# Kernel optimization log

Measured on AMD Instinct MI355X. Metric: run time of the kernel, lower is better.

The kernel has to match this reference:

```python
import jax, jax.numpy as jnp
import numpy as np

D_MODEL = 1024
N_HEADS = 16
D_HEAD = D_MODEL // N_HEADS
B, T = 2, 2048


def setup_inputs() -> dict:
    key = jax.random.key(0)
    k1, k2, k3 = jax.random.split(key, 3)
    x = jax.random.normal(k1, (B, T, D_MODEL), dtype=jnp.float32)
    # torch nn.Linear weights: y = x @ W.T, W has shape [out, in]
    W_qkv = jax.random.normal(k2, (3 * D_MODEL, D_MODEL), dtype=jnp.float32) * (1.0 / np.sqrt(D_MODEL))
    W_out = jax.random.normal(k3, (D_MODEL, D_MODEL), dtype=jnp.float32) * (1.0 / np.sqrt(D_MODEL))
    return {"x": x, "W_qkv": W_qkv, "W_out": W_out}


def reference(x, W_qkv, W_out):
    Bb, Tt, Dd = x.shape
    qkv = (x @ W_qkv.T).reshape(Bb, Tt, 3, N_HEADS, D_HEAD)
    q, k, v = qkv[:, :, 0], qkv[:, :, 1], qkv[:, :, 2]  # [B,T,H,d]
    q = q.transpose(0, 2, 1, 3)  # [B,H,T,d]
    k = k.transpose(0, 2, 1, 3)
    v = v.transpose(0, 2, 1, 3)
    scale = 1.0 / np.sqrt(D_HEAD)
    scores = jnp.einsum('bhqd,bhkd->bhqk', q, k) * scale  # [B,H,T,T]
    causal = jnp.tril(jnp.ones((Tt, Tt), dtype=bool))
    scores = jnp.where(causal, scores, -jnp.inf)
    A = jax.nn.softmax(scores, axis=-1)
    AV = jnp.einsum('bhqk,bhkd->bhqd', A, v)
    AAV = jnp.einsum('bhqk,bhkd->bhqd', A, AV)  # twicing correction
    out = 2.0 * AV - AAV  # [B,H,T,d]
    out = out.transpose(0, 2, 1, 3).reshape(Bb, Tt, Dd)
    return out @ W_out.T
```

## Files before the change

### kernel.cpp

```cpp
#include <hip/hip_runtime.h>
#include <hip/hip_bf16.h>

#define T_SEQ  2048
#define DMODEL 1024
#define NH     16
#define DH     64
#define NTOK   4096
#define QSCALE 0.18033688011112042f
#define M_FIX  16.0f

typedef unsigned short u16;
typedef short s16x8 __attribute__((ext_vector_type(8)));
typedef unsigned short u16x8 __attribute__((ext_vector_type(8)));
typedef float f32x4 __attribute__((ext_vector_type(4)));

__device__ __forceinline__ u16 f2bf(float f) {
  unsigned u = __float_as_uint(f);
  u += 0x7FFFu + ((u >> 16) & 1u);
  return (u16)(u >> 16);
}
__device__ __forceinline__ unsigned pk2(float a, float b) {
  __hip_bfloat162 h = __float22bfloat162_rn(make_float2(a, b));
  unsigned u;
  __builtin_memcpy(&u, &h, 4);
  return u;
}
__device__ __forceinline__ unsigned pk2z(float a, float b) {
  return __builtin_amdgcn_perm(__float_as_uint(b), __float_as_uint(a), 0x07060302);
}
__device__ __forceinline__ float bf2f(u16 x) {
  return __uint_as_float(((unsigned)x) << 16);
}
__device__ __forceinline__ void async_cp16(const u16* g, u16* l) {
  __builtin_amdgcn_global_load_lds(
      (const __attribute__((address_space(1))) unsigned*)g,
      (__attribute__((address_space(3))) unsigned*)l, 16, 0, 0);
}

__global__ void cast_all(const float* __restrict__ x, const float* __restrict__ wqkv,
                         const float* __restrict__ wout, u16* __restrict__ out) {
  int i = blockIdx.x * blockDim.x + threadIdx.x;
  const float* src; int off;
  if (i < 1048576)      { src = x;    off = 0; }
  else if (i < 1835008) { src = wqkv; off = 1048576; }
  else                  { src = wout; off = 1835008; }
  float4 v = reinterpret_cast<const float4*>(src)[i - off];
  ushort4 r;
  r.x = f2bf(v.x); r.y = f2bf(v.y); r.z = f2bf(v.z); r.w = f2bf(v.w);
  reinterpret_cast<ushort4*>(out)[i] = r;
}

__global__ __launch_bounds__(512, 2) void gemm_qkv(
    const u16* __restrict__ A, const u16* __restrict__ Bm,
    u16* __restrict__ outQ, u16* __restrict__ outK, u16* __restrict__ outV) {
  __shared__ __align__(16) u16 SM[57344];
  const int tid = threadIdx.x, wave = tid >> 6, lane = tid & 63;
  const int f15 = lane & 15, quad = lane >> 4;
  const int bm = blockIdx.x * 256, bn = blockIdx.y * 192;
  const int wm = wave >> 2, wn = wave & 3;
  const int K = DMODEL;

  f32x4 acc[8][3] = {};

  const u16* Ag0 = A + (size_t)(bm + (2 * wave) * 16 + f15) * K + quad * 8;
  const u16* Ag1 = A + (size_t)(bm + (2 * wave + 1) * 16 + f15) * K + quad * 8;
  const int bf0 = (wave < 4) ? (2 * wave) : (wave + 4);
  const int bf1 = 2 * wave + 1;
  const u16* Bg0 = Bm + (size_t)(bn + bf0 * 16 + f15) * K + quad * 8;
  const u16* Bg1 = Bm + (size_t)(bn + bf1 * 16 + f15) * K + quad * 8;
  u16* LA0 = SM + (2 * wave) * 512 + lane * 8;
  u16* LA1 = SM + (2 * wave + 1) * 512 + lane * 8;
  u16* LB0 = SM + 8192 + bf0 * 512 + lane * 8;
  u16* LB1 = SM + 8192 + bf1 * 512 + lane * 8;

#define QKV_STAGE(s_) do { \
    const int k0_ = (s_) * 32, o_ = ((s_) & 3) * 14336; \
    async_cp16(Ag0 + k0_, LA0 + o_); async_cp16(Ag1 + k0_, LA1 + o_); \
    async_cp16(Bg0 + k0_, LB0 + o_); \
    if (wave < 4) async_cp16(Bg1 + k0_, LB1 + o_); \
  } while (0)

  const int S = K >> 5;
  QKV_STAGE(0); QKV_STAGE(1); QKV_STAGE(2);

  for (int s = 0; s < S; s++) {
    if (s < S - 2) {
      if (wave < 4) asm volatile("s_waitcnt vmcnt(8)" ::: "memory");
      else          asm volatile("s_waitcnt vmcnt(6)" ::: "memory");
    } else if (s == S - 2) {
      if (wave < 4) asm volatile("s_waitcnt vmcnt(4)" ::: "memory");
      else          asm volatile("s_waitcnt vmcnt(3)" ::: "memory");
    } else {
      asm volatile("s_waitcnt vmcnt(0)" ::: "memory");
    }
    __builtin_amdgcn_s_barrier();
    __builtin_amdgcn_sched_barrier(0);
    if (s + 3 < S) QKV_STAGE(s + 3);
    const u16* Sl = SM + (s & 3) * 14336;
    s16x8 af[8], bfr[3];
#pragma unroll
    for (int ni = 0; ni < 3; ni++)
      bfr[ni] = *reinterpret_cast<const s16x8*>(Sl + 8192 + (wn * 3 + ni) * 512 + lane * 8);
#pragma unroll
    for (int mi = 0; mi < 8; mi++)
      af[mi] = *reinterpret_cast<const s16x8*>(Sl + (wm * 8 + mi) * 512 + lane * 8);
    __builtin_amdgcn_s_setprio(1);
#pragma unroll
    for (int mi = 0; mi < 8; mi++)
#pragma unroll
      for (int ni = 0; ni < 3; ni++)
        acc[mi][ni] = __builtin_amdgcn_mfma_f32_16x16x32_bf16(af[mi], bfr[ni], acc[mi][ni], 0, 0, 0);
    __builtin_amdgcn_s_setprio(0);
  }
#undef QKV_STAGE

  __syncthreads();
  u16* Cs = SM;
  const int ST = 200;
  const bool hasQK = (bn < 2048);
  const bool hasV  = (bn + 192 > 2048);
#pragma unroll
  for (int c = 0; c < 4; c++) {
    if (c) __syncthreads();
    if (wm == (c >> 1)) {
#pragma unroll
      for (int mi2 = 0; mi2 < 4; mi2++) {
        const int mi = (c & 1) * 4 + mi2;
#pragma unroll
        for (int ni = 0; ni < 3; ni++) {
          const int col = (wn * 3 + ni) * 16 + f15;
          const float sc = (bn + col < 1024) ? QSCALE : 1.0f;
#pragma unroll
          for (int r = 0; r < 4; r++)
            Cs[(mi2 * 16 + quad * 4 + r) * ST + col] = f2bf(acc[mi][ni][r] * sc);
        }
      }
    }
    __syncthreads();
    if (hasQK) {
      const int row = tid >> 3, cs = (tid & 7) * 24;
      const int gm = bm + c * 64 + row;
#pragma unroll
      for (int c8 = 0; c8 < 3; c8++) {
        const int gc = bn + cs + c8 * 8;
        if (gc < 2048) {
          u16x8 v = *reinterpret_cast<const u16x8*>(&Cs[row * ST + cs + c8 * 8]);
          const int which = gc >> 10, hh = (gc >> 6) & 15, d = gc & 63;
          u16* dst = (which ? outK : outQ) + ((size_t)hh * NTOK + gm) * 64 + d;
          *reinterpret_cast<u16x8*>(dst) = v;
        }
      }
    }
    if (hasV) {
      const int fc = tid >> 3, s8 = (tid & 7) * 8;
      const int tb = ((s8 >> 5) & 1) * 32 + ((s8 >> 3) & 3) * 4;
      const int gmb = bm + c * 64;
#pragma unroll
      for (int p = 0; p < 3; p++) {
        const int d = p * 64 + fc;
        const int gcd = bn + d;
        if (gcd >= 2048) {
          u16x8 vv;
#pragma unroll
          for (int j = 0; j < 4; j++) vv[j] = Cs[(tb + j) * ST + d];
#pragma unroll
          for (int j = 0; j < 4; j++) vv[4 + j] = Cs[(tb + 16 + j) * ST + d];
          *reinterpret_cast<u16x8*>(outV + (size_t)(gcd - 2048) * NTOK + gmb + s8) = vv;
        }
      }
    }
  }
}

__global__ __launch_bounds__(256) void gemm_out(
    const u16* __restrict__ A, const u16* __restrict__ Bm, float* __restrict__ outF) {
  __shared__ __align__(16) u16 SM[18432];
  const int tid = threadIdx.x, wave = tid >> 6, lane = tid & 63;
  const int f15 = lane & 15, quad = lane >> 4;
  const int bm = blockIdx.x * 64, bn = blockIdx.y * 128;
  const int wr = wave >> 1, wc = wave & 1;
  const int K = DMODEL, N = DMODEL;

  f32x4 acc[2][4] = {};

  const u16* Ag = A  + (size_t)(bm + wave * 16 + f15) * K + quad * 8;
  const u16* Bg0 = Bm + (size_t)(bn + (2 * wave) * 16 + f15) * K + quad * 8;
  const u16* Bg1 = Bm + (size_t)(bn + (2 * wave + 1) * 16 + f15) * K + quad * 8;
  u16* LA  = SM + wave * 512 + lane * 8;
  u16* LB0 = SM + 2048 + (2 * wave) * 512 + lane * 8;
  u16* LB1 = SM + 2048 + (2 * wave + 1) * 512 + lane * 8;

  const int KT = K >> 5;
  async_cp16(Ag, LA); async_cp16(Bg0, LB0); async_cp16(Bg1, LB1);
  async_cp16(Ag + 32, LA + 6144); async_cp16(Bg0 + 32, LB0 + 6144); async_cp16(Bg1 + 32, LB1 + 6144);

  int bufr = 0, bufw = 2;
  for (int kt = 0; kt < KT; kt++) {
    if (kt + 1 < KT) asm volatile("s_waitcnt vmcnt(3)" ::: "memory");
    else             asm volatile("s_waitcnt vmcnt(0)" ::: "memory");
    __builtin_amdgcn_s_barrier();
    __builtin_amdgcn_sched_barrier(0);
    if (kt + 2 < KT) {
      const int k0 = (kt + 2) * 32;
      const int o = bufw * 6144;
      async_cp16(Ag + k0, LA + o); async_cp16(Bg0 + k0, LB0 + o); async_cp16(Bg1 + k0, LB1 + o);
    }
    const u16* Af = SM + bufr * 6144;
    const u16* Bf = Af + 2048;
    s16x8 af[2], bfr[4];
#pragma unroll
    for (int mi = 0; mi < 2; mi++)
      af[mi] = *reinterpret_cast<const s16x8*>(Af + (wr * 2 + mi) * 512 + lane * 8);
#pragma unroll
    for (int ni = 0; ni < 4; ni++)
      bfr[ni] = *reinterpret_cast<const s16x8*>(Bf + (wc * 4 + ni) * 512 + lane * 8);
#pragma unroll
    for (int mi = 0; mi < 2; mi++)
#pragma unroll
      for (int ni = 0; ni < 4; ni++)
        acc[mi][ni] = __builtin_amdgcn_mfma_f32_16x16x32_bf16(af[mi], bfr[ni], acc[mi][ni], 0, 0, 0);
    bufr = (bufr == 2) ? 0 : bufr + 1;
    bufw = (bufw == 2) ? 0 : bufw + 1;
  }

#pragma unroll
  for (int mi = 0; mi < 2; mi++)
#pragma unroll
    for (int ni = 0; ni < 4; ni++)
#pragma unroll
      for (int r = 0; r < 4; r++)
        outF[(size_t)(bm + wr * 32 + mi * 16 + quad * 4 + r) * N + bn + wc * 64 + ni * 16 + f15] =
            acc[mi][ni][r];
}

template <int PASS>
__global__ __launch_bounds__(256) void attn_pass(
    const u16* __restrict__ Qb, const u16* __restrict__ Kb, const u16* __restrict__ Vsrc,
    float* __restrict__ LinvG, u16* __restrict__ Vp2, u16* __restrict__ TW) {
  __shared__ __align__(16) u16 SM[16384];
  const int tid = threadIdx.x, wave = tid >> 6, lane = tid & 63;
  const int f15 = lane & 15, quad = lane >> 4;
  const int bid = blockIdx.x;
  const int y = (bid & 7) * 4 + ((bid >> 3) & 3);
  const int b = y >> 4, h = y & 15;
  const int g = bid >> 5;
  const int qt2 = (g < 8) ? (15 - g) : (g - 8);
  const int q0 = qt2 * 128;
  const int ntiles = 2 * qt2 + 2;
  const size_t qk_base = ((size_t)h * NTOK + (size_t)b * T_SEQ) * 64;
  const size_t vt_base = (size_t)h * 64 * NTOK + (size_t)b * T_SEQ;

  s16x8 qf[2][2];
#pragma unroll
  for (int grp = 0; grp < 2; grp++) {
    const u16* qp = Qb + qk_base + (size_t)(q0 + 32 * wave + 16 * grp + f15) * 64 + quad * 8;
    qf[grp][0] = *reinterpret_cast<const s16x8*>(qp);
    qf[grp][1] = *reinterpret_cast<const s16x8*>(qp + 32);
  }
  float invl[2] = {0.f, 0.f};
  if (PASS == 1) {
#pragma unroll
    for (int grp = 0; grp < 2; grp++)
      invl[grp] = LinvG[(size_t)y * T_SEQ + q0 + 32 * wave + 16 * grp + f15];
  }

  f32x4 accO[2][4] = {};
  float l_acc[2] = {0.f, 0.f};

  const u16* Kg = Kb  + qk_base + (size_t)(wave * 16 + f15) * 64 + quad * 8;
  const u16* Vg = Vsrc + vt_base + (size_t)(wave * 16 + f15) * NTOK + quad * 8;
  u16* LK = SM + (wave * 2) * 512 + lane * 8;
  u16* LV = SM + 4096 + (wave * 2) * 512 + lane * 8;

  async_cp16(Kg, LK); async_cp16(Kg + 32, LK + 512);
  async_cp16(Vg, LV); async_cp16(Vg + 32, LV + 512);
  __syncthreads();

  for (int ti = 0; ti < ntiles; ti++) {
    const int buf = ti & 1;
    if (ti + 1 < ntiles) {
      const int j1 = (ti + 1) * 64;
      const int o = (buf ^ 1) * 8192;
      async_cp16(Kg + (size_t)j1 * 64, LK + o);
      async_cp16(Kg + (size_t)j1 * 64 + 32, LK + o + 512);
      async_cp16(Vg + j1, LV + o);
      async_cp16(Vg + j1 + 32, LV + o + 512);
    }
    const u16* Kf = SM + buf * 8192;
    const u16* Vf = SM + buf * 8192 + 4096;
    const int D = (ti - 2 * qt2) * 64;

    if (D < 32 * wave + 32) {
      f32x4 accS[2][4] = {};
#pragma unroll
      for (int st = 0; st < 4; st++) {
        s16x8 k0 = *reinterpret_cast<const s16x8*>(Kf + (st * 2) * 512 + lane * 8);
        s16x8 k1 = *reinterpret_cast<const s16x8*>(Kf + (st * 2 + 1) * 512 + lane * 8);
#pragma unroll
        for (int grp = 0; grp < 2; grp++) {
          accS[grp][st] = __builtin_amdgcn_mfma_f32_16x16x32_bf16(k0, qf[grp][0], accS[grp][st], 0, 0, 0);
          accS[grp][st] = __builtin_amdgcn_mfma_f32_16x16x32_bf16(k1, qf[grp][1], accS[grp][st], 0, 0, 0);
        }
      }
      union pbu { s16x8 v; unsigned u[4]; } pb[2][2];
      if (D + 63 <= 32 * wave) {
#pragma unroll
        for (int grp = 0; grp < 2; grp++)
#pragma unroll
          for (int st = 0; st < 4; st++) {
            float e0 = __builtin_amdgcn_exp2f(accS[grp][st][0] - M_FIX);
            float e1 = __builtin_amdgcn_exp2f(accS[grp][st][1] - M_FIX);
            float e2 = __builtin_amdgcn_exp2f(accS[grp][st][2] - M_FIX);
            float e3 = __builtin_amdgcn_exp2f(accS[grp][st][3] - M_FIX);
            if (PASS == 0) l_acc[grp] += (e0 + e1) + (e2 + e3);
            unsigned w0 = pk2z(e0, e1), w1 = pk2z(e2, e3);
            if (st < 2) { pb[grp][0].u[(st & 1) * 2] = w0; pb[grp][0].u[(st & 1) * 2 + 1] = w1; }
            else        { pb[grp][1].u[(st & 1) * 2] = w0; pb[grp][1].u[(st & 1) * 2 + 1] = w1; }
          }
      } else {
#pragma unroll
        for (int grp = 0; grp < 2; grp++) {
          const int qrel = 32 * wave + 16 * grp + f15;
#pragma unroll
          for (int st = 0; st < 4; st++) {
            const int jb = D + st * 16 + quad * 4;
            float e0 = (jb + 0 <= qrel) ? __builtin_amdgcn_exp2f(accS[grp][st][0] - M_FIX) : 0.f;
            float e1 = (jb + 1 <= qrel) ? __builtin_amdgcn_exp2f(accS[grp][st][1] - M_FIX) : 0.f;
            float e2 = (jb + 2 <= qrel) ? __builtin_amdgcn_exp2f(accS[grp][st][2] - M_FIX) : 0.f;
            float e3 = (jb + 3 <= qrel) ? __builtin_amdgcn_exp2f(accS[grp][st][3] - M_FIX) : 0.f;
            if (PASS == 0) l_acc[grp] += (e0 + e1) + (e2 + e3);
            unsigned w0 = pk2z(e0, e1), w1 = pk2z(e2, e3);
            if (st < 2) { pb[grp][0].u[(st & 1) * 2] = w0; pb[grp][0].u[(st & 1) * 2 + 1] = w1; }
            else        { pb[grp][1].u[(st & 1) * 2] = w0; pb[grp][1].u[(st & 1) * 2 + 1] = w1; }
          }
        }
      }
#pragma unroll
      for (int mt = 0; mt < 4; mt++) {
        s16x8 v0 = *reinterpret_cast<const s16x8*>(Vf + (mt * 2) * 512 + lane * 8);
        s16x8 v1 = *reinterpret_cast<const s16x8*>(Vf + (mt * 2 + 1) * 512 + lane * 8);
#pragma unroll
        for (int grp = 0; grp < 2; grp++) {
          accO[grp][mt] = __builtin_amdgcn_mfma_f32_16x16x32_bf16(v0, pb[grp][0].v, accO[grp][mt], 0, 0, 0);
          accO[grp][mt] = __builtin_amdgcn_mfma_f32_16x16x32_bf16(v1, pb[grp][1].v, accO[grp][mt], 0, 0, 0);
        }
      }
    }
    __syncthreads();
  }

  if (PASS == 0) {
#pragma unroll
    for (int grp = 0; grp < 2; grp++) {
      float l = l_acc[grp];
      l += __shfl_xor(l, 16);
      l += __shfl_xor(l, 32);
      invl[grp] = 1.0f / l;
      if (quad == 0) LinvG[(size_t)y * T_SEQ + q0 + 32 * wave + 16 * grp + f15] = invl[grp];
    }
  }

  if (PASS == 0) {
    u16* E = SM;
#pragma unroll
    for (int g64 = 0; g64 < 2; g64++) {
      __syncthreads();
      if ((wave >> 1) == g64) {
#pragma unroll
        for (int grp = 0; grp < 2; grp++) {
          const int ql = 32 * (wave & 1) + 16 * grp + f15;
          const int slot = (ql >> 5) * 32 + ((ql >> 2) & 3) * 8 + ((ql >> 4) & 1) * 4 + (ql & 3);
#pragma unroll
          for (int mt = 0; mt < 4; mt++)
#pragma unroll
            for (int r = 0; r < 4; r++)
              E[(mt * 16 + quad * 4 + r) * 68 + slot] = f2bf(accO[grp][mt][r] * invl[grp]);
        }
      }
      __syncthreads();
      const int d = tid >> 2, s = (tid & 3) * 16;
      const u16* vg2 = Vsrc + vt_base + (size_t)d * NTOK + q0 + 64 * g64 + s;
      u16* og = Vp2 + vt_base + (size_t)d * NTOK + q0 + 64 * g64 + s;
#pragma unroll
      for (int g2 = 0; g2 < 2; g2++) {
        u16x8 vv = *reinterpret_cast<const u16x8*>(vg2 + g2 * 8);
        u16x8 ee = *reinterpret_cast<const u16x8*>(&E[d * 68 + s + g2 * 8]);
        u16x8 oo;
#pragma unroll
        for (int i = 0; i < 8; i++) oo[i] = f2bf(2.0f * bf2f(vv[i]) - bf2f(ee[i]));
        *reinterpret_cast<u16x8*>(og + g2 * 8) = oo;
      }
    }
  } else {
    u16* E2 = SM;
#pragma unroll
    for (int g64 = 0; g64 < 2; g64++) {
      __syncthreads();
      if ((wave >> 1) == g64) {
#pragma unroll
        for (int grp = 0; grp < 2; grp++) {
          const int ql = 32 * (wave & 1) + 16 * grp + f15;
#pragma unroll
          for (int mt = 0; mt < 4; mt++) {
            uint2 w;
            w.x = pk2(accO[grp][mt][0] * invl[grp], accO[grp][mt][1] * invl[grp]);
            w.y = pk2(accO[grp][mt][2] * invl[grp], accO[grp][mt][3] * invl[grp]);
            *reinterpret_cast<uint2*>(&E2[ql * 72 + mt * 16 + quad * 4]) = w;
          }
        }
      }
      __syncthreads();
      const int q = tid >> 2, s = (tid & 3) * 16;
      u16* dst = TW + ((size_t)b * T_SEQ + q0 + 64 * g64 + q) * DMODEL + h * 64 + s;
      *reinterpret_cast<u16x8*>(dst) = *reinterpret_cast<const u16x8*>(&E2[q * 72 + s]);
      *reinterpret_cast<u16x8*>(dst + 8) = *reinterpret_cast<const u16x8*>(&E2[q * 72 + s + 8]);
    }
  }
}

extern "C" void kernel_launch(void* const* d_in, const int* in_sizes, int n_in,
                              void* d_out, int out_size, void* d_ws, size_t ws_size,
                              hipStream_t stream) {
  const float* x    = (const float*)d_in[0];
  const float* Wqkv = (const float*)d_in[1];
  const float* Wout = (const float*)d_in[2];
  float* out = (float*)d_out;
  char* ws = (char*)d_ws;

  u16*   Xb    = (u16*)(ws + 0);
  u16*   Wqkvb = (u16*)(ws + 8388608);
  u16*   Woutb = (u16*)(ws + 14680064);
  u16*   Qb    = (u16*)(ws + 16777216);
  u16*   Kb    = (u16*)(ws + 25165824);
  u16*   Vtp   = (u16*)(ws + 33554432);
  u16*   TW    = (u16*)(ws + 41943040);
  u16*   Vp2   = (u16*)(ws + 50331648);
  float* LinvG = (float*)(ws + 58720256);

  cast_all<<<8192, 256, 0, stream>>>(x, Wqkv, Wout, Xb);

  gemm_qkv<<<dim3(16, 16), 512, 0, stream>>>(Xb, Wqkvb, Qb, Kb, Vtp);

  attn_pass<0><<<512, 256, 0, stream>>>(Qb, Kb, Vtp, LinvG, Vp2, nullptr);
  attn_pass<1><<<512, 256, 0, stream>>>(Qb, Kb, Vp2, LinvG, nullptr, TW);

  gemm_out<<<dim3(64, 8), 256, 0, stream>>>(TW, Woutb, out);
}
```

Before: 216.1 us.

## Load K/V fragments directly from global memory instead of double-buffered LDS

Drops the shared-memory double-buffered async copy of K and V tiles and the per-tile block barrier. Each wave now loads its MFMA K and V fragments straight from global memory into registers and skips fully masked tiles with a per-wave continue. This removes the LDS traffic and __syncthreads stalls. In exchange, the 4 waves re-read the same K/V data from global memory or cache, and there is no explicit prefetch to hide load latency.

After: 269.5 us. 24.7% more time.

```diff
diff --git a/kernel.cpp b/kernel.cpp
--- a/kernel.cpp
+++ b/kernel.cpp
@@ -267,86 +267,76 @@
   f32x4 accO[2][4] = {};
   float l_acc[2] = {0.f, 0.f};
 
-  const u16* Kg = Kb  + qk_base + (size_t)(wave * 16 + f15) * 64 + quad * 8;
-  const u16* Vg = Vsrc + vt_base + (size_t)(wave * 16 + f15) * NTOK + quad * 8;
-  u16* LK = SM + (wave * 2) * 512 + lane * 8;
-  u16* LV = SM + 4096 + (wave * 2) * 512 + lane * 8;
-
-  async_cp16(Kg, LK); async_cp16(Kg + 32, LK + 512);
-  async_cp16(Vg, LV); async_cp16(Vg + 32, LV + 512);
-  __syncthreads();
+  const u16* KgB = Kb   + qk_base + (size_t)f15 * 64 + quad * 8;
+  const u16* VgB = Vsrc + vt_base + (size_t)f15 * NTOK + quad * 8;
 
   for (int ti = 0; ti < ntiles; ti++) {
-    const int buf = ti & 1;
-    if (ti + 1 < ntiles) {
-      const int j1 = (ti + 1) * 64;
-      const int o = (buf ^ 1) * 8192;
-      async_cp16(Kg + (size_t)j1 * 64, LK + o);
-      async_cp16(Kg + (size_t)j1 * 64 + 32, LK + o + 512);
-      async_cp16(Vg + j1, LV + o);
-      async_cp16(Vg + j1 + 32, LV + o + 512);
-    }
-    const u16* Kf = SM + buf * 8192;
-    const u16* Vf = SM + buf * 8192 + 4096;
     const int D = (ti - 2 * qt2) * 64;
-
-    if (D < 32 * wave + 32) {
-      f32x4 accS[2][4] = {};
-#pragma unroll
-      for (int st = 0; st < 4; st++) {
-        s16x8 k0 = *reinterpret_cast<const s16x8*>(Kf + (st * 2) * 512 + lane * 8);
-        s16x8 k1 = *reinterpret_cast<const s16x8*>(Kf + (st * 2 + 1) * 512 + lane * 8);
-#pragma unroll
-        for (int grp = 0; grp < 2; grp++) {
-          accS[grp][st] = __builtin_amdgcn_mfma_f32_16x16x32_bf16(k0, qf[grp][0], accS[grp][st], 0, 0, 0);
-          accS[grp][st] = __builtin_amdgcn_mfma_f32_16x16x32_bf16(k1, qf[grp][1], accS[grp][st], 0, 0, 0);
-        }
-      }
-      union pbu { s16x8 v; unsigned u[4]; } pb[2][2];
-      if (D + 63 <= 32 * wave) {
-#pragma unroll
-        for (int grp = 0; grp < 2; grp++)
-#pragma unroll
-          for (int st = 0; st < 4; st++) {
-            float e0 = __builtin_amdgcn_exp2f(accS[grp][st][0] - M_FIX);
-            float e1 = __builtin_amdgcn_exp2f(accS[grp][st][1] - M_FIX);
-            float e2 = __builtin_amdgcn_exp2f(accS[grp][st][2] - M_FIX);
-            float e3 = __builtin_amdgcn_exp2f(accS[grp][st][3] - M_FIX);
-            if (PASS == 0) l_acc[grp] += (e0 + e1) + (e2 + e3);
-            unsigned w0 = pk2z(e0, e1), w1 = pk2z(e2, e3);
-            if (st < 2) { pb[grp][0].u[(st & 1) * 2] = w0; pb[grp][0].u[(st & 1) * 2 + 1] = w1; }
-            else        { pb[grp][1].u[(st & 1) * 2] = w0; pb[grp][1].u[(st & 1) * 2 + 1] = w1; }
-          }
-      } else {
-#pragma unroll
-        for (int grp = 0; grp < 2; grp++) {
-          const int qrel = 32 * wave + 16 * grp + f15;
-#pragma unroll
-          for (int st = 0; st < 4; st++) {
-            const int jb = D + st * 16 + quad * 4;
-            float e0 = (jb + 0 <= qrel) ? __builtin_amdgcn_exp2f(accS[grp][st][0] - M_FIX) : 0.f;
-            float e1 = (jb + 1 <= qrel) ? __builtin_amdgcn_exp2f(accS[grp][st][1] - M_FIX) : 0.f;
-            float e2 = (jb + 2 <= qrel) ? __builtin_amdgcn_exp2f(accS[grp][st][2] - M_FIX) : 0.f;
-            float e3 = (jb + 3 <= qrel) ? __builtin_amdgcn_exp2f(accS[grp][st][3] - M_FIX) : 0.f;
-            if (PASS == 0) l_acc[grp] += (e0 + e1) + (e2 + e3);
-            unsigned w0 = pk2z(e0, e1), w1 = pk2z(e2, e3);
-            if (st < 2) { pb[grp][0].u[(st & 1) * 2] = w0; pb[grp][0].u[(st & 1) * 2 + 1] = w1; }
-            else        { pb[grp][1].u[(st & 1) * 2] = w0; pb[grp][1].u[(st & 1) * 2 + 1] = w1; }
-          }
-        }
-      }
-#pragma unroll
-      for (int mt = 0; mt < 4; mt++) {
-        s16x8 v0 = *reinterpret_cast<const s16x8*>(Vf + (mt * 2) * 512 + lane * 8);
-        s16x8 v1 = *reinterpret_cast<const s16x8*>(Vf + (mt * 2 + 1) * 512 + lane * 8);
-#pragma unroll
-        for (int grp = 0; grp < 2; grp++) {
-          accO[grp][mt] = __builtin_amdgcn_mfma_f32_16x16x32_bf16(v0, pb[grp][0].v, accO[grp][mt], 0, 0, 0);
-          accO[grp][mt] = __builtin_amdgcn_mfma_f32_16x16x32_bf16(v1, pb[grp][1].v, accO[grp][mt], 0, 0, 0);
-        }
-      }
-    }
-    __syncthreads();
+    if (D >= 32 * wave + 32) continue;
+    const int j = ti * 64;
+
+    s16x8 kf[4][2], vf[4][2];
+#pragma unroll
+    for (int st = 0; st < 4; st++) {
+      kf[st][0] = *reinterpret_cast<const s16x8*>(KgB + (size_t)(j + st * 16) * 64);
+      kf[st][1] = *reinterpret_cast<const s16x8*>(KgB + (size_t)(j + st * 16) * 64 + 32);
+    }
+#pragma unroll
+    for (int mt = 0; mt < 4; mt++) {
+      vf[mt][0] = *reinterpret_cast<const s16x8*>(VgB + (size_t)(mt * 16) * NTOK + j);
+      vf[mt][1] = *reinterpret_cast<const s16x8*>(VgB + (size_t)(mt * 16) * NTOK + j + 32);
+    }
+
+    f32x4 accS[2][4] = {};
+#pragma unroll
+    for (int st = 0; st < 4; st++) {
+#pragma unroll
+      for (int grp = 0; grp < 2; grp++) {
+        accS[grp][st] = __builtin_amdgcn_mfma_f32_16x16x32_bf16(kf[st][0], qf[grp][0], accS[grp][st], 0, 0, 0);
+        accS[grp][st] = __builtin_amdgcn_mfma_f32_16x16x32_bf16(kf[st][1], qf[grp][1], accS[grp][st], 0, 0, 0);
+      }
+    }
+    union pbu { s16x8 v; unsigned u[4]; } pb[2][2];
+    if (D + 63 <= 32 * wave) {
+#pragma unroll
+      for (int grp = 0; grp < 2; grp++)
+#pragma unroll
+        for (int st = 0; st < 4; st++) {
+          float e0 = __builtin_amdgcn_exp2f(accS[grp][st][0] - M_FIX);
+          float e1 = __builtin_amdgcn_exp2f(accS[grp][st][1] - M_FIX);
+          float e2 = __builtin_amdgcn_exp2f(accS[grp][st][2] - M_FIX);
+          float e3 = __builtin_amdgcn_exp2f(accS[grp][st][3] - M_FIX);
+          if (PASS == 0) l_acc[grp] += (e0 + e1) + (e2 + e3);
+          unsigned w0 = pk2z(e0, e1), w1 = pk2z(e2, e3);
+          if (st < 2) { pb[grp][0].u[(st & 1) * 2] = w0; pb[grp][0].u[(st & 1) * 2 + 1] = w1; }
+          else        { pb[grp][1].u[(st & 1) * 2] = w0; pb[grp][1].u[(st & 1) * 2 + 1] = w1; }
+        }
+    } else {
+#pragma unroll
+      for (int grp = 0; grp < 2; grp++) {
+        const int qrel = 32 * wave + 16 * grp + f15;
+#pragma unroll
+        for (int st = 0; st < 4; st++) {
+          const int jb = D + st * 16 + quad * 4;
+          float e0 = (jb + 0 <= qrel) ? __builtin_amdgcn_exp2f(accS[grp][st][0] - M_FIX) : 0.f;
+          float e1 = (jb + 1 <= qrel) ? __builtin_amdgcn_exp2f(accS[grp][st][1] - M_FIX) : 0.f;
+          float e2 = (jb + 2 <= qrel) ? __builtin_amdgcn_exp2f(accS[grp][st][2] - M_FIX) : 0.f;
+          float e3 = (jb + 3 <= qrel) ? __builtin_amdgcn_exp2f(accS[grp][st][3] - M_FIX) : 0.f;
+          if (PASS == 0) l_acc[grp] += (e0 + e1) + (e2 + e3);
+          unsigned w0 = pk2z(e0, e1), w1 = pk2z(e2, e3);
+          if (st < 2) { pb[grp][0].u[(st & 1) * 2] = w0; pb[grp][0].u[(st & 1) * 2 + 1] = w1; }
+          else        { pb[grp][1].u[(st & 1) * 2] = w0; pb[grp][1].u[(st & 1) * 2 + 1] = w1; }
+        }
+      }
+    }
+#pragma unroll
+    for (int mt = 0; mt < 4; mt++) {
+#pragma unroll
+      for (int grp = 0; grp < 2; grp++) {
+        accO[grp][mt] = __builtin_amdgcn_mfma_f32_16x16x32_bf16(vf[mt][0], pb[grp][0].v, accO[grp][mt], 0, 0, 0);
+        accO[grp][mt] = __builtin_amdgcn_mfma_f32_16x16x32_bf16(vf[mt][1], pb[grp][1].v, accO[grp][mt], 0, 0, 0);
+      }
+    }
   }
 
   if (PASS == 0) {
```

## Enlarge output GEMM tile to 128x128 with 8 waves and 4-stage pipeline

Applied to the files above, without the earlier changes.

The output projection GEMM now uses 128x128 block tiles computed by 512 threads (8 waves in a 2x4 grid), up from 64x128 tiles on 256 threads. The LDS ring grows from 3 to 4 stages, and each wave issues one A and one B async copy per stage. MFMA sections are wrapped in s_setprio. The aim is better operand reuse per block and deeper latency hiding. In exchange the launch has half as many blocks (256) and uses more LDS per block.

New measurement: 208.0 us. 1.04x faster.

```diff
diff --git a/kernel.cpp b/kernel.cpp
--- a/kernel.cpp
+++ b/kernel.cpp
@@ -172,64 +172,62 @@
   }
 }
 
-__global__ __launch_bounds__(256) void gemm_out(
+__global__ __launch_bounds__(512, 2) void gemm_out(
     const u16* __restrict__ A, const u16* __restrict__ Bm, float* __restrict__ outF) {
-  __shared__ __align__(16) u16 SM[18432];
+  __shared__ __align__(16) u16 SM[32768];
   const int tid = threadIdx.x, wave = tid >> 6, lane = tid & 63;
   const int f15 = lane & 15, quad = lane >> 4;
-  const int bm = blockIdx.x * 64, bn = blockIdx.y * 128;
-  const int wr = wave >> 1, wc = wave & 1;
+  const int bm = blockIdx.x * 128, bn = blockIdx.y * 128;
+  const int wm = wave >> 2, wn = wave & 3;
   const int K = DMODEL, N = DMODEL;
 
-  f32x4 acc[2][4] = {};
+  f32x4 acc[4][2] = {};
 
   const u16* Ag = A  + (size_t)(bm + wave * 16 + f15) * K + quad * 8;
-  const u16* Bg0 = Bm + (size_t)(bn + (2 * wave) * 16 + f15) * K + quad * 8;
-  const u16* Bg1 = Bm + (size_t)(bn + (2 * wave + 1) * 16 + f15) * K + quad * 8;
-  u16* LA  = SM + wave * 512 + lane * 8;
-  u16* LB0 = SM + 2048 + (2 * wave) * 512 + lane * 8;
-  u16* LB1 = SM + 2048 + (2 * wave + 1) * 512 + lane * 8;
-
-  const int KT = K >> 5;
-  async_cp16(Ag, LA); async_cp16(Bg0, LB0); async_cp16(Bg1, LB1);
-  async_cp16(Ag + 32, LA + 6144); async_cp16(Bg0 + 32, LB0 + 6144); async_cp16(Bg1 + 32, LB1 + 6144);
-
-  int bufr = 0, bufw = 2;
-  for (int kt = 0; kt < KT; kt++) {
-    if (kt + 1 < KT) asm volatile("s_waitcnt vmcnt(3)" ::: "memory");
-    else             asm volatile("s_waitcnt vmcnt(0)" ::: "memory");
+  const u16* Bg = Bm + (size_t)(bn + wave * 16 + f15) * K + quad * 8;
+  u16* LA = SM + wave * 512 + lane * 8;
+  u16* LB = SM + 4096 + wave * 512 + lane * 8;
+
+#define OUT_STAGE(s_) do { \
+    const int k0_ = (s_) * 32, o_ = ((s_) & 3) * 8192; \
+    async_cp16(Ag + k0_, LA + o_); async_cp16(Bg + k0_, LB + o_); \
+  } while (0)
+
+  const int S = K >> 5;
+  OUT_STAGE(0); OUT_STAGE(1); OUT_STAGE(2);
+
+  for (int s = 0; s < S; s++) {
+    if (s < S - 2)       asm volatile("s_waitcnt vmcnt(4)" ::: "memory");
+    else if (s == S - 2) asm volatile("s_waitcnt vmcnt(2)" ::: "memory");
+    else                 asm volatile("s_waitcnt vmcnt(0)" ::: "memory");
     __builtin_amdgcn_s_barrier();
     __builtin_amdgcn_sched_barrier(0);
-    if (kt + 2 < KT) {
-      const int k0 = (kt + 2) * 32;
-      const int o = bufw * 6144;
-      async_cp16(Ag + k0, LA + o); async_cp16(Bg0 + k0, LB0 + o); async_cp16(Bg1 + k0, LB1 + o);
-    }
-    const u16* Af = SM + bufr * 6144;
-    const u16* Bf = Af + 2048;
-    s16x8 af[2], bfr[4];
-#pragma unroll
-    for (int mi = 0; mi < 2; mi++)
-      af[mi] = *reinterpret_cast<const s16x8*>(Af + (wr * 2 + mi) * 512 + lane * 8);
-#pragma unroll
-    for (int ni = 0; ni < 4; ni++)
-      bfr[ni] = *reinterpret_cast<const s16x8*>(Bf + (wc * 4 + ni) * 512 + lane * 8);
-#pragma unroll
-    for (int mi = 0; mi < 2; mi++)
-#pragma unroll
-      for (int ni = 0; ni < 4; ni++)
+    if (s + 3 < S) OUT_STAGE(s + 3);
+    const u16* Sl = SM + (s & 3) * 8192;
+    s16x8 af[4], bfr[2];
+#pragma unroll
+    for (int ni = 0; ni < 2; ni++)
+      bfr[ni] = *reinterpret_cast<const s16x8*>(Sl + 4096 + (wn * 2 + ni) * 512 + lane * 8);
+#pragma unroll
+    for (int mi = 0; mi < 4; mi++)
+      af[mi] = *reinterpret_cast<const s16x8*>(Sl + (wm * 4 + mi) * 512 + lane * 8);
+    __builtin_amdgcn_s_setprio(1);
+#pragma unroll
+    for (int mi = 0; mi < 4; mi++)
+#pragma unroll
+      for (int ni = 0; ni < 2; ni++)
         acc[mi][ni] = __builtin_amdgcn_mfma_f32_16x16x32_bf16(af[mi], bfr[ni], acc[mi][ni], 0, 0, 0);
-    bufr = (bufr == 2) ? 0 : bufr + 1;
-    bufw = (bufw == 2) ? 0 : bufw + 1;
-  }
-
-#pragma unroll
-  for (int mi = 0; mi < 2; mi++)
-#pragma unroll
-    for (int ni = 0; ni < 4; ni++)
+    __builtin_amdgcn_s_setprio(0);
+  }
+#undef OUT_STAGE
+
+#pragma unroll
+  for (int mi = 0; mi < 4; mi++)
+#pragma unroll
+    for (int ni = 0; ni < 2; ni++)
 #pragma unroll
       for (int r = 0; r < 4; r++)
-        outF[(size_t)(bm + wr * 32 + mi * 16 + quad * 4 + r) * N + bn + wc * 64 + ni * 16 + f15] =
+        outF[(size_t)(bm + wm * 64 + mi * 16 + quad * 4 + r) * N + bn + wn * 32 + ni * 16 + f15] =
             acc[mi][ni][r];
 }
 
@@ -444,5 +442,5 @@
   attn_pass<0><<<512, 256, 0, stream>>>(Qb, Kb, Vtp, LinvG, Vp2, nullptr);
   attn_pass<1><<<512, 256, 0, stream>>>(Qb, Kb, Vp2, LinvG, nullptr, TW);
 
-  gemm_out<<<dim3(64, 8), 256, 0, stream>>>(TW, Woutb, out);
-}
+  gemm_out<<<dim3(32, 8), 512, 0, stream>>>(TW, Woutb, out);
+}
```
